# Optimization experiments

Hardware: AMD Instinct MI355X
Metric: run time of the kernel (lower is better)

The kernel has to match this reference:

```python
import jax, jax.numpy as jnp
import numpy as np
import math

H, W = 128, 128
FOV_X = 60.0
OPACITY_SCALE = 1.0
T_STOP = 1e-3  # early-termination threshold from the source (transmittance.max() < 0.001)
N_GAUSS = 2048


def setup_inputs() -> dict:
    key = jax.random.key(0)
    ks = jax.random.split(key, 6)
    N = N_GAUSS
    # place Gaussians in front of the camera so they rasterize (view_matrix = identity)
    xy = jax.random.uniform(ks[0], (N, 2), minval=-1.5, maxval=1.5, dtype=jnp.float32)
    z = jax.random.uniform(ks[1], (N, 1), minval=2.0, maxval=6.0, dtype=jnp.float32)
    positions = jnp.concatenate([xy, z], axis=1)
    scales = jax.random.uniform(ks[2], (N, 3), minval=0.02, maxval=0.08, dtype=jnp.float32)
    rotations = jax.random.normal(ks[3], (N, 4), dtype=jnp.float32)
    colors = jax.random.uniform(ks[4], (N, 3), dtype=jnp.float32)
    opacities = jax.random.uniform(ks[5], (N,), dtype=jnp.float32) * 0.9
    view_matrix = jnp.eye(4, dtype=jnp.float32)
    return {"positions": positions, "scales": scales, "rotations": rotations,
            "colors": colors, "opacities": opacities, "view_matrix": view_matrix}


def _preprocess(positions, scales, rotations, view_matrix):
    # quaternion (w,x,y,z) -> rotation matrix, same entry layout as the torch source
    q = rotations / (jnp.linalg.norm(rotations, axis=1, keepdims=True) + 1e-8)
    w, x, y, z = q[:, 0], q[:, 1], q[:, 2], q[:, 3]
    r00 = 1 - 2 * (y * y + z * z); r01 = 2 * (x * y + z * w); r02 = 2 * (x * z - y * w)
    r10 = 2 * (x * y - z * w); r11 = 1 - 2 * (x * x + z * z); r12 = 2 * (y * z + x * w)
    r20 = 2 * (x * z + y * w); r21 = 2 * (y * z - x * w); r22 = 1 - 2 * (x * x + y * y)
    Rm = jnp.stack([jnp.stack([r00, r01, r02], -1),
                    jnp.stack([r10, r11, r12], -1),
                    jnp.stack([r20, r21, r22], -1)], 1)  # (N,3,3)
    s2 = jnp.maximum(scales, 1e-6) ** 2
    # cov3d[i,k] = sum_j R[i,j] * s2[j] * R[k,j]
    cov3d = jnp.einsum('nij,nj,nkj->nik', Rm, s2, Rm)

    Rv = view_matrix[:3, :3]; tv = view_matrix[:3, 3]
    pos_cam = positions @ Rv.T + tv[None, :]
    X, Y, Z = pos_cam[:, 0], pos_cam[:, 1], pos_cam[:, 2]
    depths = Z
    valid = (Z > 0.1).astype(jnp.float32)

    fx = W / 2 / math.tan(math.radians(FOV_X) / 2)
    fy = fx
    Zs = jnp.maximum(Z, 1e-6)
    means_2d = jnp.stack([fx * X / Zs + W / 2, fy * Y / Zs + H / 2], 1)

    # projection Jacobian rows (N,3)
    invZ2 = 1.0 / Zs ** 2
    zeros = jnp.zeros_like(Zs)
    J0 = jnp.stack([fx / Zs, zeros, -fx * X * invZ2], 1)
    J1 = jnp.stack([zeros, fy / Zs, -fy * Y * invZ2], 1)
    SRt0 = jnp.einsum('nij,j->ni', cov3d, Rv[0])
    SRt1 = jnp.einsum('nij,j->ni', cov3d, Rv[1])
    c00 = jnp.sum(J0 * SRt0, 1)
    c01 = jnp.sum(J0 * SRt1, 1)
    c11 = jnp.sum(J1 * SRt1, 1)

    # radii from eigenvalue BEFORE the 1e-6 eye regularization (as in source)
    tr = c00 + c11
    det = c00 * c11 - c01 ** 2
    disc = jnp.maximum(tr ** 2 - 4 * det, 0.0)
    lam = (tr + jnp.sqrt(disc)) / 2.0
    radii = 3.0 * jnp.sqrt(jnp.maximum(lam, 1e-8))
    c00 = c00 + 1e-6
    c11 = c11 + 1e-6
    return means_2d, c00, c01, c11, depths, radii, valid


def _render(means_2d, c00, c01, c11, colors, opacities, depths, radii):
    # depth sort descending, exactly as torch.argsort(depths, descending=True)
    order = jnp.argsort(-depths)
    mu = means_2d[order]; col = colors[order]; op = opacities[order]; r = radii[order]
    c00 = c00[order]; c01 = c01[order]; c11 = c11[order]
    det = c00 * c11 - c01 ** 2 + 1e-8
    ic00 = (c11 / det)[:, None, None]
    ic01 = (-c01 / det)[:, None, None]
    ic11 = (c00 / det)[:, None, None]

    px = jnp.arange(W, dtype=jnp.float32)[None, None, :]   # (1,1,W)
    py = jnp.arange(H, dtype=jnp.float32)[None, :, None]   # (1,H,1)
    mux = mu[:, 0][:, None, None]; muy = mu[:, 1][:, None, None]
    rb = r[:, None, None]
    # bbox via int() truncation semantics of the source
    px_min = jnp.maximum(0.0, jnp.trunc(mux - rb)); px_max = jnp.minimum(float(W), jnp.trunc(mux + rb) + 1)
    py_min = jnp.maximum(0.0, jnp.trunc(muy - rb)); py_max = jnp.minimum(float(H), jnp.trunc(muy + rb) + 1)
    mask = (px >= px_min) & (px < px_max) & (py >= py_min) & (py < py_max)  # (N,H,W)

    dx = px - mux; dy = py - muy
    expo = -0.5 * (ic00 * dx * dx + 2 * ic01 * dx * dy + ic11 * dy * dy)
    G = jnp.exp(jnp.minimum(expo, 0.0))
    alpha = op[:, None, None] * G * mask  # (N,H,W), zero outside bbox (matching 'continue')

    # front-to-back transmittance product: T_i = prod_{j<i} (1 - alpha_j)
    T = jnp.cumprod(1.0 - alpha, axis=0)
    T_excl = jnp.concatenate([jnp.ones((1, H, W), alpha.dtype), T[:-1]], axis=0)
    # emulate the early break: splats processed only while max T >= 1e-3 (monotone)
    active = (jnp.max(T_excl, axis=(1, 2)) >= T_STOP).astype(alpha.dtype)
    weight = alpha * T_excl * active[:, None, None]
    image = jnp.einsum('nhw,nc->hwc', weight, col)  # (H,W,3)
    return image


def reference(positions, scales, rotations, colors, opacities, view_matrix):
    means_2d, c00, c01, c11, depths, radii, valid = _preprocess(positions, scales, rotations, view_matrix)
    op = opacities * OPACITY_SCALE * valid
    return _render(means_2d, c00, c01, c11, colors, op, depths, radii)
```

## Files before the change

### kernel.cpp

```cpp
#include <hip/hip_runtime.h>
#include <math.h>

#define NG 2048
#define WIMG 128
#define HIMG 128
#define REC 12
#define SEG 16
#define RTILE 8
#define GPB 4


__global__ void __launch_bounds__(256)
preprocess_kernel(const float* __restrict__ pos,
                  const float* __restrict__ scales,
                  const float* __restrict__ rot,
                  const float* __restrict__ colors,
                  const float* __restrict__ opac,
                  const float* __restrict__ view,
                  float* __restrict__ srec,
                  int N)
{
    __shared__ float ps[NG * 3];
    __shared__ float zs[NG];
    const int t = threadIdx.x;

    for (int j = t; j < 3 * N; j += 256) ps[j] = pos[j];
    __syncthreads();

    const float Rv20 = view[8], Rv21 = view[9], Rv22 = view[10], tv2 = view[11];
    for (int j = t; j < N; j += 256) {
        zs[j] = Rv20 * ps[3*j] + Rv21 * ps[3*j+1] + Rv22 * ps[3*j+2] + tv2;
    }
    __syncthreads();

    const int wid = t >> 6, lane = t & 63;
    const int i = blockIdx.x * GPB + wid;
    if (i >= N) return;

    const float di = zs[i];
    int cnt = 0;
    for (int j = lane; j < N; j += 64) {
        float dj = zs[j];
        cnt += (dj > di) || (dj == di && j < i);
    }
    #pragma unroll
    for (int off = 32; off; off >>= 1) cnt += __shfl_xor(cnt, off);
    const int rank = cnt;

    float qw = rot[4*i+0], qx = rot[4*i+1], qy = rot[4*i+2], qz = rot[4*i+3];
    float nrm = sqrtf(qw*qw + qx*qx + qy*qy + qz*qz) + 1e-8f;
    qw /= nrm; qx /= nrm; qy /= nrm; qz /= nrm;
    float R[3][3];
    R[0][0] = 1.f - 2.f*(qy*qy + qz*qz); R[0][1] = 2.f*(qx*qy + qz*qw); R[0][2] = 2.f*(qx*qz - qy*qw);
    R[1][0] = 2.f*(qx*qy - qz*qw); R[1][1] = 1.f - 2.f*(qx*qx + qz*qz); R[1][2] = 2.f*(qy*qz + qx*qw);
    R[2][0] = 2.f*(qx*qz + qy*qw); R[2][1] = 2.f*(qy*qz - qx*qw); R[2][2] = 1.f - 2.f*(qx*qx + qy*qy);

    float sv[3];
    sv[0] = fmaxf(scales[3*i+0], 1e-6f); sv[0] *= sv[0];
    sv[1] = fmaxf(scales[3*i+1], 1e-6f); sv[1] *= sv[1];
    sv[2] = fmaxf(scales[3*i+2], 1e-6f); sv[2] *= sv[2];

    float C[3][3];
    #pragma unroll
    for (int a = 0; a < 3; ++a)
        #pragma unroll
        for (int b = 0; b < 3; ++b)
            C[a][b] = R[a][0]*sv[0]*R[b][0] + R[a][1]*sv[1]*R[b][1] + R[a][2]*sv[2]*R[b][2];

    float Rv[3][3], tv[3];
    #pragma unroll
    for (int r = 0; r < 3; ++r) {
        Rv[r][0] = view[4*r+0]; Rv[r][1] = view[4*r+1]; Rv[r][2] = view[4*r+2];
        tv[r] = view[4*r+3];
    }
    float Px = ps[3*i], Py = ps[3*i+1], Pz = ps[3*i+2];
    float X = Rv[0][0]*Px + Rv[0][1]*Py + Rv[0][2]*Pz + tv[0];
    float Y = Rv[1][0]*Px + Rv[1][1]*Py + Rv[1][2]*Pz + tv[1];
    float Z = di;

    float valid = (Z > 0.1f) ? 1.f : 0.f;
    float Zs = fmaxf(Z, 1e-6f);
    const float fx = 110.85125168440814f;
    float mux = fx * X / Zs + 64.f;
    float muy = fx * Y / Zs + 64.f;
    float invZ2 = 1.f / (Zs * Zs);
    float J0[3] = { fx / Zs, 0.f, -fx * X * invZ2 };
    float J1[3] = { 0.f, fx / Zs, -fx * Y * invZ2 };

    float SRt0[3], SRt1[3];
    #pragma unroll
    for (int a = 0; a < 3; ++a) {
        SRt0[a] = C[a][0]*Rv[0][0] + C[a][1]*Rv[0][1] + C[a][2]*Rv[0][2];
        SRt1[a] = C[a][0]*Rv[1][0] + C[a][1]*Rv[1][1] + C[a][2]*Rv[1][2];
    }
    float c00 = J0[0]*SRt0[0] + J0[1]*SRt0[1] + J0[2]*SRt0[2];
    float c01 = J0[0]*SRt1[0] + J0[1]*SRt1[1] + J0[2]*SRt1[2];
    float c11 = J1[0]*SRt1[0] + J1[1]*SRt1[1] + J1[2]*SRt1[2];

    float trc = c00 + c11;
    float det = c00 * c11 - c01 * c01;
    float disc = fmaxf(trc*trc - 4.f*det, 0.f);
    float lam = 0.5f * (trc + sqrtf(disc));
    float rad = 3.f * sqrtf(fmaxf(lam, 1e-8f));
    c00 += 1e-6f; c11 += 1e-6f;
    float det2 = c00 * c11 - c01 * c01 + 1e-8f;
    float ic00 = c11 / det2, ic01 = -c01 / det2, ic11 = c00 / det2;
    float opv = opac[i] * valid;

    float pxmin = fmaxf(0.f,   truncf(mux - rad));
    float pxmax = fminf(128.f, truncf(mux + rad) + 1.f);
    float pymin = fmaxf(0.f,   truncf(muy - rad));
    float pymax = fminf(128.f, truncf(muy + rad) + 1.f);

    int ixmin = (int)fminf(pxmin, 255.f);
    int ixmax = (int)fmaxf(pxmax, 0.f);
    int iymin = (int)fminf(pymin, 255.f);
    int iymax = (int)fmaxf(pymax, 0.f);
    unsigned int bbox = (unsigned)ixmin | ((unsigned)ixmax << 8)
                      | ((unsigned)iymin << 16) | ((unsigned)iymax << 24);

    if (lane == 0) {
        float4* o = (float4*)(srec + (size_t)rank * REC);
        o[0] = make_float4(mux, muy, ic00, ic01);
        o[1] = make_float4(ic11, opv, colors[3*i+0], colors[3*i+1]);
        o[2] = make_float4(colors[3*i+2], di, __uint_as_float(bbox), 0.f);
    }
}

__global__ void __launch_bounds__(1024)
render_kernel(const float* __restrict__ srec, float* __restrict__ out, int N)
{
    __shared__ float4 part[SEG][64];
    const int t    = threadIdx.x;
    const int lane = t & 63;
    const int seg  = t >> 6;
    const int tilesX = WIMG / RTILE;
    const int tileX = blockIdx.x % tilesX;
    const int tileY = blockIdx.x / tilesX;
    const int x = tileX * RTILE + (lane & (RTILE - 1));
    const int y = tileY * RTILE + (lane / RTILE);
    const float fpx = (float)x, fpy = (float)y;
    const int tx0 = tileX * RTILE, tx1 = tx0 + RTILE;
    const int ty0 = tileY * RTILE, ty1 = ty0 + RTILE;

    const int chunk = (N + SEG - 1) / SEG;
    const int k0 = seg * chunk;
    const int k1 = min(k0 + chunk, N);

    float T = 1.f, aR = 0.f, aG = 0.f, aB = 0.f;
    const float4* rec = (const float4*)srec;

    for (int base = k0; base < k1; base += 64) {
        const int g = base + lane;
        float4 r0 = make_float4(0,0,0,0), r1 = r0, r2 = r0;
        bool hit = false;
        if (g < k1) {
            r0 = rec[g*3+0];
            r1 = rec[g*3+1];
            r2 = rec[g*3+2];
            unsigned bb = __float_as_uint(r2.z);
            int xmin = bb & 255, xmax = (bb >> 8) & 255;
            int ymin = (bb >> 16) & 255, ymax = bb >> 24;
            hit = (xmin < tx1) && (xmax > tx0) && (ymin < ty1) && (ymax > ty0);
        }
        unsigned long long m = __ballot(hit);
        while (m) {
            const int b = __ffsll((long long)m) - 1;
            m &= m - 1;
            float mux = __shfl(r0.x, b), muy = __shfl(r0.y, b);
            float i00 = __shfl(r0.z, b), i01 = __shfl(r0.w, b);
            float i11 = __shfl(r1.x, b), op  = __shfl(r1.y, b);
            float c0  = __shfl(r1.z, b), c1  = __shfl(r1.w, b);
            float c2  = __shfl(r2.x, b);
            unsigned bb = __float_as_uint(__shfl(r2.z, b));
            int xmin = bb & 255, xmax = (bb >> 8) & 255;
            int ymin = (bb >> 16) & 255, ymax = bb >> 24;
            bool inside = (x >= xmin) && (x < xmax) && (y >= ymin) && (y < ymax);
            float dx = fpx - mux, dy = fpy - muy;
            float e = -0.5f * (i00*dx*dx + 2.f*i01*dx*dy + i11*dy*dy);
            float G = __expf(fminf(e, 0.f));
            float alpha = inside ? (op * G) : 0.f;
            float w = alpha * T;
            aR += w * c0;
            aG += w * c1;
            aB += w * c2;
            T *= (1.f - alpha);
        }
    }

    part[seg][lane] = make_float4(aR, aG, aB, T);
    __syncthreads();

    if (t < 64) {
        float accR = 0.f, accG = 0.f, accB = 0.f, Tacc = 1.f;
        #pragma unroll
        for (int s = 0; s < SEG; ++s) {
            float4 p = part[s][t];
            accR += Tacc * p.x;
            accG += Tacc * p.y;
            accB += Tacc * p.z;
            Tacc *= p.w;
        }
        int idx = (y * WIMG + x) * 3;
        out[idx+0] = accR;
        out[idx+1] = accG;
        out[idx+2] = accB;
    }
}

extern "C" void kernel_launch(void* const* d_in, const int* in_sizes, int n_in,
                              void* d_out, int out_size, void* d_ws, size_t ws_size,
                              hipStream_t stream) {
    const float* pos    = (const float*)d_in[0];
    const float* scales = (const float*)d_in[1];
    const float* rot    = (const float*)d_in[2];
    const float* colors = (const float*)d_in[3];
    const float* opac   = (const float*)d_in[4];
    const float* view   = (const float*)d_in[5];
    float* out = (float*)d_out;
    float* srec = (float*)d_ws;
    const int N = in_sizes[4];

    const int nPreBlocks = (N + GPB - 1) / GPB;
    preprocess_kernel<<<nPreBlocks, 256, 0, stream>>>(
        pos, scales, rot, colors, opac, view, srec, N);

    const int nTiles = (WIMG / RTILE) * (HIMG / RTILE);
    render_kernel<<<nTiles, 1024, 0, stream>>>(srec, out, N);
}
```

Measured before the change: 16.35 us.

## Fuse preprocess and render into one cooperative kernel with grid sync

Merges the preprocessing kernel and the tile renderer into a single kernel launched with hipLaunchCooperativeKernel. A grid-wide barrier separates the stages. Each of the 256 1024-thread blocks projects and depth-ranks 8 Gaussians and then renders its 8x8 tile. Positions are now read directly from global memory instead of being staged in LDS. This removes the second launch and the gap between kernels, in exchange for the cost of a grid barrier. It also requires every block to be co-resident, and only half the waves do preprocessing work.

```diff
diff --git a/kernel.cpp b/kernel.cpp
--- a/kernel.cpp
+++ b/kernel.cpp
@@ -1,4 +1,5 @@
 #include <hip/hip_runtime.h>
+#include <hip/hip_cooperative_groups.h>
 #include <math.h>
 
 #define NG 2048
@@ -7,133 +8,131 @@
 #define REC 12
 #define SEG 16
 #define RTILE 8
-#define GPB 4
-
-
-__global__ void __launch_bounds__(256)
-preprocess_kernel(const float* __restrict__ pos,
-                  const float* __restrict__ scales,
-                  const float* __restrict__ rot,
-                  const float* __restrict__ colors,
-                  const float* __restrict__ opac,
-                  const float* __restrict__ view,
-                  float* __restrict__ srec,
-                  int N)
+#define GPB 8
+
+
+__global__ void __launch_bounds__(1024)
+fused_kernel(const float* __restrict__ pos,
+             const float* __restrict__ scales,
+             const float* __restrict__ rot,
+             const float* __restrict__ colors,
+             const float* __restrict__ opac,
+             const float* __restrict__ view,
+             float* __restrict__ srec,
+             float* __restrict__ out,
+             int N)
 {
-    __shared__ float ps[NG * 3];
+    namespace cg = cooperative_groups;
+    cg::grid_group gg = cg::this_grid();
+
     __shared__ float zs[NG];
+    __shared__ float4 part[SEG][64];
+
     const int t = threadIdx.x;
-
-    for (int j = t; j < 3 * N; j += 256) ps[j] = pos[j];
+    const int wid = t >> 6, lane = t & 63;
+
+    {
+        const float Rv20 = view[8], Rv21 = view[9], Rv22 = view[10], tv2 = view[11];
+        for (int j = t; j < N; j += 1024) {
+            zs[j] = Rv20 * pos[3*j] + Rv21 * pos[3*j+1] + Rv22 * pos[3*j+2] + tv2;
+        }
+    }
     __syncthreads();
 
-    const float Rv20 = view[8], Rv21 = view[9], Rv22 = view[10], tv2 = view[11];
-    for (int j = t; j < N; j += 256) {
-        zs[j] = Rv20 * ps[3*j] + Rv21 * ps[3*j+1] + Rv22 * ps[3*j+2] + tv2;
-    }
-    __syncthreads();
-
-    const int wid = t >> 6, lane = t & 63;
     const int i = blockIdx.x * GPB + wid;
-    if (i >= N) return;
-
-    const float di = zs[i];
-    int cnt = 0;
-    for (int j = lane; j < N; j += 64) {
-        float dj = zs[j];
-        cnt += (dj > di) || (dj == di && j < i);
-    }
-    #pragma unroll
-    for (int off = 32; off; off >>= 1) cnt += __shfl_xor(cnt, off);
-    const int rank = cnt;
-
-    float qw = rot[4*i+0], qx = rot[4*i+1], qy = rot[4*i+2], qz = rot[4*i+3];
-    float nrm = sqrtf(qw*qw + qx*qx + qy*qy + qz*qz) + 1e-8f;
-    qw /= nrm; qx /= nrm; qy /= nrm; qz /= nrm;
-    float R[3][3];
-    R[0][0] = 1.f - 2.f*(qy*qy + qz*qz); R[0][1] = 2.f*(qx*qy + qz*qw); R[0][2] = 2.f*(qx*qz - qy*qw);
-    R[1][0] = 2.f*(qx*qy - qz*qw); R[1][1] = 1.f - 2.f*(qx*qx + qz*qz); R[1][2] = 2.f*(qy*qz + qx*qw);
-    R[2][0] = 2.f*(qx*qz + qy*qw); R[2][1] = 2.f*(qy*qz - qx*qw); R[2][2] = 1.f - 2.f*(qx*qx + qy*qy);
-
-    float sv[3];
-    sv[0] = fmaxf(scales[3*i+0], 1e-6f); sv[0] *= sv[0];
-    sv[1] = fmaxf(scales[3*i+1], 1e-6f); sv[1] *= sv[1];
-    sv[2] = fmaxf(scales[3*i+2], 1e-6f); sv[2] *= sv[2];
-
-    float C[3][3];
-    #pragma unroll
-    for (int a = 0; a < 3; ++a)
-        #pragma unroll
-        for (int b = 0; b < 3; ++b)
-            C[a][b] = R[a][0]*sv[0]*R[b][0] + R[a][1]*sv[1]*R[b][1] + R[a][2]*sv[2]*R[b][2];
-
-    float Rv[3][3], tv[3];
-    #pragma unroll
-    for (int r = 0; r < 3; ++r) {
-        Rv[r][0] = view[4*r+0]; Rv[r][1] = view[4*r+1]; Rv[r][2] = view[4*r+2];
-        tv[r] = view[4*r+3];
-    }
-    float Px = ps[3*i], Py = ps[3*i+1], Pz = ps[3*i+2];
-    float X = Rv[0][0]*Px + Rv[0][1]*Py + Rv[0][2]*Pz + tv[0];
-    float Y = Rv[1][0]*Px + Rv[1][1]*Py + Rv[1][2]*Pz + tv[1];
-    float Z = di;
-
-    float valid = (Z > 0.1f) ? 1.f : 0.f;
-    float Zs = fmaxf(Z, 1e-6f);
-    const float fx = 110.85125168440814f;
-    float mux = fx * X / Zs + 64.f;
-    float muy = fx * Y / Zs + 64.f;
-    float invZ2 = 1.f / (Zs * Zs);
-    float J0[3] = { fx / Zs, 0.f, -fx * X * invZ2 };
-    float J1[3] = { 0.f, fx / Zs, -fx * Y * invZ2 };
-
-    float SRt0[3], SRt1[3];
-    #pragma unroll
-    for (int a = 0; a < 3; ++a) {
-        SRt0[a] = C[a][0]*Rv[0][0] + C[a][1]*Rv[0][1] + C[a][2]*Rv[0][2];
-        SRt1[a] = C[a][0]*Rv[1][0] + C[a][1]*Rv[1][1] + C[a][2]*Rv[1][2];
-    }
-    float c00 = J0[0]*SRt0[0] + J0[1]*SRt0[1] + J0[2]*SRt0[2];
-    float c01 = J0[0]*SRt1[0] + J0[1]*SRt1[1] + J0[2]*SRt1[2];
-    float c11 = J1[0]*SRt1[0] + J1[1]*SRt1[1] + J1[2]*SRt1[2];
-
-    float trc = c00 + c11;
-    float det = c00 * c11 - c01 * c01;
-    float disc = fmaxf(trc*trc - 4.f*det, 0.f);
-    float lam = 0.5f * (trc + sqrtf(disc));
-    float rad = 3.f * sqrtf(fmaxf(lam, 1e-8f));
-    c00 += 1e-6f; c11 += 1e-6f;
-    float det2 = c00 * c11 - c01 * c01 + 1e-8f;
-    float ic00 = c11 / det2, ic01 = -c01 / det2, ic11 = c00 / det2;
-    float opv = opac[i] * valid;
-
-    float pxmin = fmaxf(0.f,   truncf(mux - rad));
-    float pxmax = fminf(128.f, truncf(mux + rad) + 1.f);
-    float pymin = fmaxf(0.f,   truncf(muy - rad));
-    float pymax = fminf(128.f, truncf(muy + rad) + 1.f);
-
-    int ixmin = (int)fminf(pxmin, 255.f);
-    int ixmax = (int)fmaxf(pxmax, 0.f);
-    int iymin = (int)fminf(pymin, 255.f);
-    int iymax = (int)fmaxf(pymax, 0.f);
-    unsigned int bbox = (unsigned)ixmin | ((unsigned)ixmax << 8)
-                      | ((unsigned)iymin << 16) | ((unsigned)iymax << 24);
-
-    if (lane == 0) {
-        float4* o = (float4*)(srec + (size_t)rank * REC);
-        o[0] = make_float4(mux, muy, ic00, ic01);
-        o[1] = make_float4(ic11, opv, colors[3*i+0], colors[3*i+1]);
-        o[2] = make_float4(colors[3*i+2], di, __uint_as_float(bbox), 0.f);
-    }
-}
-
-__global__ void __launch_bounds__(1024)
-render_kernel(const float* __restrict__ srec, float* __restrict__ out, int N)
-{
-    __shared__ float4 part[SEG][64];
-    const int t    = threadIdx.x;
-    const int lane = t & 63;
-    const int seg  = t >> 6;
+    if (wid < GPB && i < N) {
+        const float di = zs[i];
+        int cnt = 0;
+        for (int j = lane; j < N; j += 64) {
+            float dj = zs[j];
+            cnt += (dj > di) || (dj == di && j < i);
+        }
+        #pragma unroll
+        for (int off = 32; off; off >>= 1) cnt += __shfl_xor(cnt, off);
+        const int rank = cnt;
+
+        float qw = rot[4*i+0], qx = rot[4*i+1], qy = rot[4*i+2], qz = rot[4*i+3];
+        float nrm = sqrtf(qw*qw + qx*qx + qy*qy + qz*qz) + 1e-8f;
+        qw /= nrm; qx /= nrm; qy /= nrm; qz /= nrm;
+        float R[3][3];
+        R[0][0] = 1.f - 2.f*(qy*qy + qz*qz); R[0][1] = 2.f*(qx*qy + qz*qw); R[0][2] = 2.f*(qx*qz - qy*qw);
+        R[1][0] = 2.f*(qx*qy - qz*qw); R[1][1] = 1.f - 2.f*(qx*qx + qz*qz); R[1][2] = 2.f*(qy*qz + qx*qw);
+        R[2][0] = 2.f*(qx*qz + qy*qw); R[2][1] = 2.f*(qy*qz - qx*qw); R[2][2] = 1.f - 2.f*(qx*qx + qy*qy);
+
+        float sv[3];
+        sv[0] = fmaxf(scales[3*i+0], 1e-6f); sv[0] *= sv[0];
+        sv[1] = fmaxf(scales[3*i+1], 1e-6f); sv[1] *= sv[1];
+        sv[2] = fmaxf(scales[3*i+2], 1e-6f); sv[2] *= sv[2];
+
+        float C[3][3];
+        #pragma unroll
+        for (int a = 0; a < 3; ++a)
+            #pragma unroll
+            for (int b = 0; b < 3; ++b)
+                C[a][b] = R[a][0]*sv[0]*R[b][0] + R[a][1]*sv[1]*R[b][1] + R[a][2]*sv[2]*R[b][2];
+
+        float Rv[3][3], tv[3];
+        #pragma unroll
+        for (int r = 0; r < 3; ++r) {
+            Rv[r][0] = view[4*r+0]; Rv[r][1] = view[4*r+1]; Rv[r][2] = view[4*r+2];
+            tv[r] = view[4*r+3];
+        }
+        float Px = pos[3*i], Py = pos[3*i+1], Pz = pos[3*i+2];
+        float X = Rv[0][0]*Px + Rv[0][1]*Py + Rv[0][2]*Pz + tv[0];
+        float Y = Rv[1][0]*Px + Rv[1][1]*Py + Rv[1][2]*Pz + tv[1];
+        float Z = di;
+
+        float valid = (Z > 0.1f) ? 1.f : 0.f;
+        float Zs = fmaxf(Z, 1e-6f);
+        const float fx = 110.85125168440814f;
+        float mux = fx * X / Zs + 64.f;
+        float muy = fx * Y / Zs + 64.f;
+        float invZ2 = 1.f / (Zs * Zs);
+        float J0[3] = { fx / Zs, 0.f, -fx * X * invZ2 };
+        float J1[3] = { 0.f, fx / Zs, -fx * Y * invZ2 };
+
+        float SRt0[3], SRt1[3];
+        #pragma unroll
+        for (int a = 0; a < 3; ++a) {
+            SRt0[a] = C[a][0]*Rv[0][0] + C[a][1]*Rv[0][1] + C[a][2]*Rv[0][2];
+            SRt1[a] = C[a][0]*Rv[1][0] + C[a][1]*Rv[1][1] + C[a][2]*Rv[1][2];
+        }
+        float c00 = J0[0]*SRt0[0] + J0[1]*SRt0[1] + J0[2]*SRt0[2];
+        float c01 = J0[0]*SRt1[0] + J0[1]*SRt1[1] + J0[2]*SRt1[2];
+        float c11 = J1[0]*SRt1[0] + J1[1]*SRt1[1] + J1[2]*SRt1[2];
+
+        float trc = c00 + c11;
+        float det = c00 * c11 - c01 * c01;
+        float disc = fmaxf(trc*trc - 4.f*det, 0.f);
+        float lam = 0.5f * (trc + sqrtf(disc));
+        float rad = 3.f * sqrtf(fmaxf(lam, 1e-8f));
+        c00 += 1e-6f; c11 += 1e-6f;
+        float det2 = c00 * c11 - c01 * c01 + 1e-8f;
+        float ic00 = c11 / det2, ic01 = -c01 / det2, ic11 = c00 / det2;
+        float opv = opac[i] * valid;
+
+        float pxmin = fmaxf(0.f,   truncf(mux - rad));
+        float pxmax = fminf(128.f, truncf(mux + rad) + 1.f);
+        float pymin = fmaxf(0.f,   truncf(muy - rad));
+        float pymax = fminf(128.f, truncf(muy + rad) + 1.f);
+
+        int ixmin = (int)fminf(pxmin, 255.f);
+        int ixmax = (int)fmaxf(pxmax, 0.f);
+        int iymin = (int)fminf(pymin, 255.f);
+        int iymax = (int)fmaxf(pymax, 0.f);
+        unsigned int bbox = (unsigned)ixmin | ((unsigned)ixmax << 8)
+                          | ((unsigned)iymin << 16) | ((unsigned)iymax << 24);
+
+        if (lane == 0) {
+            float4* o = (float4*)(srec + (size_t)rank * REC);
+            o[0] = make_float4(mux, muy, ic00, ic01);
+            o[1] = make_float4(ic11, opv, colors[3*i+0], colors[3*i+1]);
+            o[2] = make_float4(colors[3*i+2], di, __uint_as_float(bbox), 0.f);
+        }
+    }
+
+    gg.sync();
+
     const int tilesX = WIMG / RTILE;
     const int tileX = blockIdx.x % tilesX;
     const int tileY = blockIdx.x / tilesX;
@@ -144,7 +143,7 @@
     const int ty0 = tileY * RTILE, ty1 = ty0 + RTILE;
 
     const int chunk = (N + SEG - 1) / SEG;
-    const int k0 = seg * chunk;
+    const int k0 = wid * chunk;
     const int k1 = min(k0 + chunk, N);
 
     float T = 1.f, aR = 0.f, aG = 0.f, aB = 0.f;
@@ -188,7 +187,7 @@
         }
     }
 
-    part[seg][lane] = make_float4(aR, aG, aB, T);
+    part[wid][lane] = make_float4(aR, aG, aB, T);
     __syncthreads();
 
     if (t < 64) {
@@ -219,12 +218,12 @@
     const float* view   = (const float*)d_in[5];
     float* out = (float*)d_out;
     float* srec = (float*)d_ws;
-    const int N = in_sizes[4];
-
-    const int nPreBlocks = (N + GPB - 1) / GPB;
-    preprocess_kernel<<<nPreBlocks, 256, 0, stream>>>(
-        pos, scales, rot, colors, opac, view, srec, N);
-
+    int N = in_sizes[4];
+
+    void* args[] = { (void*)&pos, (void*)&scales, (void*)&rot, (void*)&colors,
+                     (void*)&opac, (void*)&view, (void*)&srec, (void*)&out,
+                     (void*)&N };
     const int nTiles = (WIMG / RTILE) * (HIMG / RTILE);
-    render_kernel<<<nTiles, 1024, 0, stream>>>(srec, out, N);
+    hipLaunchCooperativeKernel((const void*)fused_kernel,
+                               dim3(nTiles), dim3(1024), args, 0, stream);
 }
```

Result: slower. 46.55 us (+184.7%).
